# Kernel tuning notes

Hardware: AMD Instinct MI355X
Metric: run time of the kernel (lower is better)

## Reference

```python
import jax, jax.numpy as jnp
import numpy as np

E = 1024   # embedding_dim
H = 16     # num_head
D = 64     # dim_head (E == H*D)
R = 8      # LoRA rank
BATCH = 2
SEQ = 2048
EPS = 1e-6


def setup_inputs() -> dict:
    key = jax.random.key(0)
    ks = jax.random.split(key, 16)
    s = 0.02
    return {
        "y": jax.random.normal(ks[0], (BATCH, SEQ, E), jnp.float32),
        "Wqkv": jax.random.normal(ks[1], (3 * E, E), jnp.float32) * s,
        "bqkv": jax.random.normal(ks[2], (3 * E,), jnp.float32) * s,
        "Wmsa": jax.random.normal(ks[3], (E, E), jnp.float32) * s,
        "Bq": jax.random.normal(ks[4], (E, R), jnp.float32) * s,
        "Aq": jax.random.normal(ks[5], (R, E), jnp.float32) * s,
        "Bk": jax.random.normal(ks[6], (E, R), jnp.float32) * s,
        "Ak": jax.random.normal(ks[7], (R, E), jnp.float32) * s,
        "Bv": jax.random.normal(ks[8], (E, R), jnp.float32) * s,
        "Av": jax.random.normal(ks[9], (R, E), jnp.float32) * s,
        "Bo": jax.random.normal(ks[10], (E, R), jnp.float32) * s,
        "Ao": jax.random.normal(ks[11], (R, E), jnp.float32) * s,
        "gamma": jnp.ones((E,), jnp.float32),
        "beta": jnp.zeros((E,), jnp.float32),
        "i": 0,
    }


def reference(y, Wqkv, bqkv, Wmsa, Bq, Aq, Bk, Ak, Bv, Av, Bo, Ao, gamma, beta, i):
    B, S, En = y.shape
    # fused QKV projection: nn.Linear -> y @ W.T + b
    qkv = (y @ Wqkv.T + bqkv).reshape(B, S, 3, H, D).transpose(2, 0, 3, 1, 4)
    Q, K, V = qkv[0], qkv[1], qkv[2]          # each [B,H,S,D]

    def lora_delta(Bw, Aw):
        # torch: y @ (B.weight @ A.weight), reshaped to heads
        return (y @ (Bw @ Aw)).reshape(B, S, H, D).transpose(0, 2, 1, 3)

    Q = Q + lora_delta(Bq, Aq)
    K = K + lora_delta(Bk, Ak)
    V = V + lora_delta(Bv, Av)

    scale = jnp.asarray(np.sqrt(D), y.dtype)
    scores = jnp.einsum('bhqd,bhkd->bhqk', Q, K) / scale
    attn = jax.nn.softmax(scores, axis=-1)
    o = jnp.einsum('bhqk,bhkd->bhqd', attn, V)          # [B,H,S,D]
    o = o.transpose(0, 2, 1, 3).reshape(B, S, H * D)    # [B,S,E]

    msa = o @ Wmsa.T + o @ (Bo @ Ao)
    res = msa + y

    mu = jnp.mean(res, axis=-1, keepdims=True)
    var = jnp.var(res, axis=-1, keepdims=True)
    return (res - mu) * jax.lax.rsqrt(var + EPS) * gamma + beta
```

## Files before the change

kernel.cpp:

```cpp
#include <hip/hip_runtime.h>
#include <hip/hip_bf16.h>
#include <stdint.h>

typedef __attribute__((ext_vector_type(8))) short short8;
typedef __attribute__((ext_vector_type(4))) float f32x4;

typedef const __attribute__((address_space(1))) void gv_t;
typedef __attribute__((address_space(3))) void lv_t;

#define SCQ 0.18033688011112042f

__device__ __forceinline__ void gl_lds16(const void* g, void* l) {
    __builtin_amdgcn_global_load_lds((gv_t*)g, (lv_t*)l, 16, 0, 0);
}

__device__ __forceinline__ unsigned short f2bf(float f) {
    union { float f; unsigned int u; } v; v.f = f;
    unsigned int r = v.u + 0x7fffu + ((v.u >> 16) & 1u);
    return (unsigned short)(r >> 16);
}

__device__ __forceinline__ unsigned int pack2bf(float a, float b) {
    union { __hip_bfloat162 h2; unsigned int u; } cv;
    cv.h2 = __float22bfloat162_rn(make_float2(a, b));
    return cv.u;
}

__device__ __forceinline__ f32x4 zero4() { f32x4 z = {0.f, 0.f, 0.f, 0.f}; return z; }

__global__ void k_prep(const float* __restrict__ y,
                       const float* __restrict__ Wqkv, const float* __restrict__ Wmsa,
                       const float* __restrict__ Bq, const float* __restrict__ Aq,
                       const float* __restrict__ Bk, const float* __restrict__ Ak,
                       const float* __restrict__ Bv, const float* __restrict__ Av,
                       const float* __restrict__ Bo, const float* __restrict__ Ao,
                       unsigned short* __restrict__ wout, unsigned short* __restrict__ yb) {
    const int bid = blockIdx.x;
    if (bid < 16384) {
        int idx = bid * 256 + threadIdx.x;
        int n = idx >> 10, k = idx & 1023;
        int sel = n >> 10, n0 = n & 1023;
        const float* Bp = (sel == 0) ? Bq : (sel == 1) ? Bk : (sel == 2) ? Bv : Bo;
        const float* Ap = (sel == 0) ? Aq : (sel == 1) ? Ak : (sel == 2) ? Av : Ao;
        float acc = (sel < 3) ? Wqkv[idx] : Wmsa[idx - 3145728];
        #pragma unroll
        for (int r = 0; r < 8; ++r) acc += Bp[k * 8 + r] * Ap[r * 1024 + n0];
        wout[idx] = f2bf(acc * ((sel == 0) ? SCQ : 1.0f));
    } else {
        int i = ((bid - 16384) * 256 + threadIdx.x) * 4;
        float4 v = *(const float4*)(y + i);
        union { unsigned short u[4]; uint2 w; } o;
        o.u[0] = f2bf(v.x); o.u[1] = f2bf(v.y); o.u[2] = f2bf(v.z); o.u[3] = f2bf(v.w);
        *(uint2*)(yb + i) = o.w;
    }
}

template <int TM, int EPI, int MINW>
__global__ __launch_bounds__(256, MINW) void k_gemm(const unsigned short* __restrict__ Ag,
                                                    const unsigned short* __restrict__ Bg,
                                                    const float* __restrict__ bias,
                                                    const float* __restrict__ yres,
                                                    unsigned short* __restrict__ vtg,
                                                    void* __restrict__ Cout,
                                                    int M, int N, int K) {
    constexpr int WAVES_N = 256 / TM;
    constexpr int WN = TM / 2;
    constexpr int NI = WN / 16;
    constexpr int ACALLS = TM / 64;
    __shared__ unsigned short As[2][TM * 32];
    __shared__ unsigned short Bs[2][128 * 32];
    const int flat = threadIdx.x;
    const int m0 = blockIdx.y * TM, n0 = blockIdx.x * 128;
    const int lane = flat & 63, wave = flat >> 6;
    const int l16 = lane & 15, quad = lane >> 4;
    const int wm = (wave / WAVES_N) * 64, wn = (wave % WAVES_N) * WN;

    f32x4 acc[4][NI];
    #pragma unroll
    for (int mi = 0; mi < 4; ++mi)
        #pragma unroll
        for (int ni = 0; ni < NI; ++ni) acc[mi][ni] = zero4();

    const unsigned short* ap = Ag + (size_t)(m0 + (flat >> 2)) * K + (flat & 3) * 8;
    const unsigned short* bp = Bg + (size_t)(n0 + (flat >> 2)) * K + (flat & 3) * 8;
    const size_t rstep = (size_t)64 * K;

    #pragma unroll
    for (int c = 0; c < ACALLS; ++c) gl_lds16(ap + c * rstep, &As[0][c * 2048 + flat * 8]);
    gl_lds16(bp,         &Bs[0][flat * 8]);
    gl_lds16(bp + rstep, &Bs[0][2048 + flat * 8]);
    ap += 32; bp += 32;
    __syncthreads();

    for (int k0 = 0; k0 < K; k0 += 32) {
        const int cur = (k0 >> 5) & 1;
        if (k0 + 32 < K) {
            const int nxt = cur ^ 1;
            #pragma unroll
            for (int c = 0; c < ACALLS; ++c) gl_lds16(ap + c * rstep, &As[nxt][c * 2048 + flat * 8]);
            gl_lds16(bp,         &Bs[nxt][flat * 8]);
            gl_lds16(bp + rstep, &Bs[nxt][2048 + flat * 8]);
            ap += 32; bp += 32;
        }

        short8 af[4], bfr[NI];
        #pragma unroll
        for (int i = 0; i < 4; ++i) af[i] = *(const short8*)&As[cur][(wm + i * 16 + l16) * 32 + quad * 8];
        #pragma unroll
        for (int i = 0; i < NI; ++i) bfr[i] = *(const short8*)&Bs[cur][(wn + i * 16 + l16) * 32 + quad * 8];
        #pragma unroll
        for (int mi = 0; mi < 4; ++mi)
            #pragma unroll
            for (int ni = 0; ni < NI; ++ni)
                acc[mi][ni] = __builtin_amdgcn_mfma_f32_16x16x32_bf16(af[mi], bfr[ni], acc[mi][ni], 0, 0, 0);

        __syncthreads();
    }

    if (EPI == 0) {
        unsigned short* C = (unsigned short*)Cout;
        if (n0 < 2048) {
            #pragma unroll
            for (int ni = 0; ni < NI; ++ni) {
                int col = n0 + wn + ni * 16 + l16;
                float bv = bias[col] * ((col < 1024) ? SCQ : 1.0f);
                #pragma unroll
                for (int mi = 0; mi < 4; ++mi) {
                    int row = m0 + wm + mi * 16 + quad * 4;
                    #pragma unroll
                    for (int r = 0; r < 4; ++r)
                        C[(size_t)(row + r) * N + col] = f2bf(acc[mi][ni][r] + bv);
                }
            }
        } else {
            #pragma unroll
            for (int ni = 0; ni < NI; ++ni) {
                int col = n0 + wn + ni * 16 + l16;
                float bv = bias[col];
                int hh = (col - 2048) >> 6, dd = col & 63;
                unsigned short* vrow0 = vtg + (size_t)(hh * 64 + dd) * 2048;
                #pragma unroll
                for (int mi = 0; mi < 4; ++mi) {
                    int row = m0 + wm + mi * 16 + quad * 4;
                    int bb = row >> 11, ss = row & 2047;
                    uint2 w;
                    w.x = pack2bf(acc[mi][ni][0] + bv, acc[mi][ni][1] + bv);
                    w.y = pack2bf(acc[mi][ni][2] + bv, acc[mi][ni][3] + bv);
                    *(uint2*)(vrow0 + (size_t)bb * 2097152 + ss) = w;
                }
            }
        }
    } else {
        float* C = (float*)Cout;
        #pragma unroll
        for (int ni = 0; ni < NI; ++ni) {
            int col = n0 + wn + ni * 16 + l16;
            #pragma unroll
            for (int mi = 0; mi < 4; ++mi) {
                int row = m0 + wm + mi * 16 + quad * 4;
                #pragma unroll
                for (int r = 0; r < 4; ++r)
                    C[(size_t)(row + r) * N + col] = acc[mi][ni][r] + yres[(size_t)(row + r) * N + col];
            }
        }
    }
}

__global__ __launch_bounds__(256, 3) void k_attn(const unsigned short* __restrict__ qkv,
                                                 const unsigned short* __restrict__ vtg,
                                                 unsigned short* __restrict__ o) {
    __shared__ unsigned short LDS[24576];
    unsigned short* Qs = LDS;
    unsigned short* Ks0 = LDS + 8192;
    unsigned short* Vt0 = LDS + 16384;

    const int t = threadIdx.x;
    const int lane = t & 63, wave = t >> 6;
    const int l16 = lane & 15, quad = lane >> 4;
    const int l8 = l16 & 7;
    const int q0 = blockIdx.x * 128;
    const int h = blockIdx.y, b = blockIdx.z;

    const unsigned short* qbase = qkv + (size_t)(b * 2048) * 3072 + h * 64;
    const unsigned short* kbase = qbase + 1024;
    const unsigned short* vtbase = vtg + (size_t)((b * 16 + h) * 64) * 2048;

    #pragma unroll
    for (int i = 0; i < 4; ++i) {
        int B = i * 256 + t;
        int row = B >> 3, c = (B & 7) ^ (row & 7);
        gl_lds16(qbase + (size_t)(q0 + row) * 3072 + c * 8, &Qs[B * 8]);
    }

    const int B0 = t, B1 = t + 256;
    const int r0 = B0 >> 3, c0 = (B0 & 7) ^ (r0 & 7);
    const int r1 = B1 >> 3, c1 = (B1 & 7) ^ (r1 & 7);
    const unsigned short* kp0 = kbase + (size_t)r0 * 3072 + c0 * 8;
    const unsigned short* kp1 = kbase + (size_t)r1 * 3072 + c1 * 8;
    const unsigned short* vp0 = vtbase + (size_t)r0 * 2048 + c0 * 8;
    const unsigned short* vp1 = vtbase + (size_t)r1 * 2048 + c1 * 8;

    gl_lds16(kp0, &Ks0[B0 * 8]);
    gl_lds16(kp1, &Ks0[B1 * 8]);
    gl_lds16(vp0, &Vt0[B0 * 8]);
    gl_lds16(vp1, &Vt0[B1 * 8]);
    kp0 += 64 * 3072; kp1 += 64 * 3072; vp0 += 64; vp1 += 64;

    __syncthreads();

    short8 qf[2][2];
    #pragma unroll
    for (int ni = 0; ni < 2; ++ni)
        #pragma unroll
        for (int kk = 0; kk < 2; ++kk)
            qf[ni][kk] = *(const short8*)&Qs[(wave * 32 + ni * 16 + l16) * 64 + ((kk * 4 + quad) ^ l8) * 8];

    f32x4 acc_o[2][4];
    #pragma unroll
    for (int mo = 0; mo < 2; ++mo)
        #pragma unroll
        for (int nd = 0; nd < 4; ++nd) acc_o[mo][nd] = zero4();
    f32x4 acc_l[2] = {zero4(), zero4()};
    short8 ones;
    #pragma unroll
    for (int i = 0; i < 8; ++i) ones[i] = (short)0x3F80;

    for (int j = 0; j < 32; ++j) {
        const unsigned short* Ks = Ks0 + (j & 1) * 4096;
        const unsigned short* Vt = Vt0 + (j & 1) * 4096;

        if (j < 31) {
            unsigned short* Kn = Ks0 + ((j + 1) & 1) * 4096;
            unsigned short* Vn = Vt0 + ((j + 1) & 1) * 4096;
            gl_lds16(kp0, &Kn[B0 * 8]);
            gl_lds16(kp1, &Kn[B1 * 8]);
            gl_lds16(vp0, &Vn[B0 * 8]);
            gl_lds16(vp1, &Vn[B1 * 8]);
            kp0 += 64 * 3072; kp1 += 64 * 3072; vp0 += 64; vp1 += 64;
        }

        f32x4 sacc[4][2];
        #pragma unroll
        for (int mi = 0; mi < 4; ++mi)
            #pragma unroll
            for (int ni = 0; ni < 2; ++ni) sacc[mi][ni] = zero4();
        #pragma unroll
        for (int kk = 0; kk < 2; ++kk)
            #pragma unroll
            for (int mi = 0; mi < 4; ++mi) {
                short8 kf = *(const short8*)&Ks[(mi * 16 + l16) * 64 + ((kk * 4 + quad) ^ l8) * 8];
                #pragma unroll
                for (int ni = 0; ni < 2; ++ni)
                    sacc[mi][ni] = __builtin_amdgcn_mfma_f32_16x16x32_bf16(kf, qf[ni][kk], sacc[mi][ni], 0, 0, 0);
            }

        short8 pf[2][2];
        #pragma unroll
        for (int ni = 0; ni < 2; ++ni)
            #pragma unroll
            for (int kk = 0; kk < 2; ++kk) {
                float e00 = __builtin_amdgcn_exp2f(sacc[2 * kk][ni][0]);
                float e01 = __builtin_amdgcn_exp2f(sacc[2 * kk][ni][1]);
                float e02 = __builtin_amdgcn_exp2f(sacc[2 * kk][ni][2]);
                float e03 = __builtin_amdgcn_exp2f(sacc[2 * kk][ni][3]);
                float e10 = __builtin_amdgcn_exp2f(sacc[2 * kk + 1][ni][0]);
                float e11 = __builtin_amdgcn_exp2f(sacc[2 * kk + 1][ni][1]);
                float e12 = __builtin_amdgcn_exp2f(sacc[2 * kk + 1][ni][2]);
                float e13 = __builtin_amdgcn_exp2f(sacc[2 * kk + 1][ni][3]);
                unsigned int a0 = pack2bf(e00, e01);
                unsigned int b0 = pack2bf(e10, e11);
                unsigned int a1 = pack2bf(e02, e03);
                unsigned int b1 = pack2bf(e12, e13);
                asm volatile("v_permlane32_swap_b32 %0, %1\n\t"
                             "v_permlane16_swap_b32 %0, %1"
                             : "+v"(a0), "+v"(b0));
                asm volatile("v_permlane32_swap_b32 %0, %1\n\t"
                             "v_permlane16_swap_b32 %0, %1"
                             : "+v"(a1), "+v"(b1));
                union { unsigned int u[4]; short8 s; } cv;
                cv.u[0] = a0; cv.u[1] = a1; cv.u[2] = b0; cv.u[3] = b1;
                pf[ni][kk] = cv.s;
            }

        #pragma unroll
        for (int kk = 0; kk < 2; ++kk) {
            #pragma unroll
            for (int mo = 0; mo < 2; ++mo)
                acc_l[mo] = __builtin_amdgcn_mfma_f32_16x16x32_bf16(pf[mo][kk], ones, acc_l[mo], 0, 0, 0);
            #pragma unroll
            for (int nd = 0; nd < 4; ++nd) {
                short8 vf = *(const short8*)&Vt[(nd * 16 + l16) * 64 + ((kk * 4 + quad) ^ l8) * 8];
                #pragma unroll
                for (int mo = 0; mo < 2; ++mo)
                    acc_o[mo][nd] = __builtin_amdgcn_mfma_f32_16x16x32_bf16(pf[mo][kk], vf, acc_o[mo][nd], 0, 0, 0);
            }
        }

        __syncthreads();
    }

    #pragma unroll
    for (int mo = 0; mo < 2; ++mo)
        #pragma unroll
        for (int rr = 0; rr < 4; ++rr) {
            float inv = 1.0f / acc_l[mo][rr];
            int qg = q0 + wave * 32 + mo * 16 + quad * 4 + rr;
            size_t base = ((size_t)(b * 2048 + qg)) * 1024 + h * 64;
            #pragma unroll
            for (int nd = 0; nd < 4; ++nd)
                o[base + nd * 16 + l16] = f2bf(acc_o[mo][nd][rr] * inv);
        }
}

__global__ __launch_bounds__(256) void k_ln(const float* __restrict__ res,
                                            const float* __restrict__ g,
                                            const float* __restrict__ be,
                                            float* __restrict__ out) {
    __shared__ float red[8];
    const int row = blockIdx.x, t = threadIdx.x;
    const float* x = res + (size_t)row * 1024;
    float4 v = *(const float4*)(x + t * 4);
    float s = v.x + v.y + v.z + v.w;
    float sq = v.x * v.x + v.y * v.y + v.z * v.z + v.w * v.w;
    #pragma unroll
    for (int off = 32; off; off >>= 1) { s += __shfl_down(s, off); sq += __shfl_down(sq, off); }
    if ((t & 63) == 0) { red[t >> 6] = s; red[4 + (t >> 6)] = sq; }
    __syncthreads();
    float ts = red[0] + red[1] + red[2] + red[3];
    float tq = red[4] + red[5] + red[6] + red[7];
    float mu = ts * (1.f / 1024.f);
    float var = tq * (1.f / 1024.f) - mu * mu;
    float rstd = rsqrtf(var + 1e-6f);
    float4 gg = *(const float4*)(g + t * 4);
    float4 bb = *(const float4*)(be + t * 4);
    float4 ov;
    ov.x = (v.x - mu) * rstd * gg.x + bb.x;
    ov.y = (v.y - mu) * rstd * gg.y + bb.y;
    ov.z = (v.z - mu) * rstd * gg.z + bb.z;
    ov.w = (v.w - mu) * rstd * gg.w + bb.w;
    *(float4*)(out + (size_t)row * 1024 + t * 4) = ov;
}

extern "C" void kernel_launch(void* const* d_in, const int* in_sizes, int n_in,
                              void* d_out, int out_size, void* d_ws, size_t ws_size,
                              hipStream_t stream) {
    (void)in_sizes; (void)n_in; (void)out_size; (void)ws_size;
    const float* y    = (const float*)d_in[0];
    const float* Wqkv = (const float*)d_in[1];
    const float* bqkv = (const float*)d_in[2];
    const float* Wmsa = (const float*)d_in[3];
    const float* Bq = (const float*)d_in[4];
    const float* Aq = (const float*)d_in[5];
    const float* Bk = (const float*)d_in[6];
    const float* Ak = (const float*)d_in[7];
    const float* Bv = (const float*)d_in[8];
    const float* Av = (const float*)d_in[9];
    const float* Bo = (const float*)d_in[10];
    const float* Ao = (const float*)d_in[11];
    const float* gamma = (const float*)d_in[12];
    const float* beta  = (const float*)d_in[13];

    char* ws = (char*)d_ws;
    unsigned short* yb   = (unsigned short*)(ws);
    unsigned short* weq  = (unsigned short*)(ws + (8u  << 20));
    unsigned short* qkv  = (unsigned short*)(ws + (16u << 20));
    unsigned short* vtg  = (unsigned short*)(ws + (40u << 20));
    unsigned short* wem  = weq + 3145728;
    unsigned short* obuf = yb;
    float* res = (float*)qkv;

    k_prep<<<17408, 256, 0, stream>>>(y, Wqkv, Wmsa, Bq, Aq, Bk, Ak, Bv, Av, Bo, Ao, weq, yb);
    k_gemm<128, 0, 3><<<dim3(24, 32), 256, 0, stream>>>(yb, weq, bqkv, nullptr, vtg, (void*)qkv, 4096, 3072, 1024);
    k_attn<<<dim3(16, 16, 2), 256, 0, stream>>>(qkv, vtg, obuf);
    k_gemm<64, 1, 4><<<dim3(8, 64), 256, 0, stream>>>(obuf, wem, nullptr, y, nullptr, (void*)res, 4096, 1024, 1024);
    k_ln  <<<4096, 256, 0, stream>>>(res, gamma, beta, (float*)d_out);
}
```

Baseline: 212.5 us.

## Split attention over two KV halves and add a partial-output reduction kernel

The attention kernel now splits the key/value sequence into two halves across extra blocks, doubling the grid. It frees LDS by reusing the Q staging area for K buffers and raises the occupancy hint from 3 to 4 blocks. Each split writes unnormalized bf16 partial outputs plus row sums, which a new reduction kernel adds, normalizes and writes out. The goal is better CU utilization at this small grid size. The cost is an extra launch, extra global traffic, and bf16 rounding of the unnormalized partial outputs.

After: 215.6 us. No clear change (+1.5%).

```diff
diff --git a/kernel.cpp b/kernel.cpp
--- a/kernel.cpp
+++ b/kernel.cpp
@@ -18,6 +18,10 @@
     union { float f; unsigned int u; } v; v.f = f;
     unsigned int r = v.u + 0x7fffu + ((v.u >> 16) & 1u);
     return (unsigned short)(r >> 16);
+}
+
+__device__ __forceinline__ float bf2f(unsigned short u) {
+    union { unsigned int i; float f; } v; v.i = ((unsigned int)u) << 16; return v.f;
 }
 
 __device__ __forceinline__ unsigned int pack2bf(float a, float b) {
@@ -166,24 +170,26 @@
     }
 }
 
-__global__ __launch_bounds__(256, 3) void k_attn(const unsigned short* __restrict__ qkv,
+__global__ __launch_bounds__(256, 4) void k_attn(const unsigned short* __restrict__ qkv,
                                                  const unsigned short* __restrict__ vtg,
-                                                 unsigned short* __restrict__ o) {
-    __shared__ unsigned short LDS[24576];
+                                                 unsigned short* __restrict__ opart,
+                                                 float* __restrict__ lout) {
+    __shared__ unsigned short LDS[16384];
     unsigned short* Qs = LDS;
-    unsigned short* Ks0 = LDS + 8192;
-    unsigned short* Vt0 = LDS + 16384;
+    unsigned short* Ks0 = LDS;
+    unsigned short* Vt0 = LDS + 8192;
 
     const int t = threadIdx.x;
     const int lane = t & 63, wave = t >> 6;
     const int l16 = lane & 15, quad = lane >> 4;
     const int l8 = l16 & 7;
     const int q0 = blockIdx.x * 128;
-    const int h = blockIdx.y, b = blockIdx.z;
+    const int h = blockIdx.y;
+    const int b = blockIdx.z >> 1, split = blockIdx.z & 1;
 
     const unsigned short* qbase = qkv + (size_t)(b * 2048) * 3072 + h * 64;
-    const unsigned short* kbase = qbase + 1024;
-    const unsigned short* vtbase = vtg + (size_t)((b * 16 + h) * 64) * 2048;
+    const unsigned short* kbase = qbase + 1024 + (size_t)(split * 1024) * 3072;
+    const unsigned short* vtbase = vtg + (size_t)((b * 16 + h) * 64) * 2048 + split * 1024;
 
     #pragma unroll
     for (int i = 0; i < 4; ++i) {
@@ -200,21 +206,23 @@
     const unsigned short* vp0 = vtbase + (size_t)r0 * 2048 + c0 * 8;
     const unsigned short* vp1 = vtbase + (size_t)r1 * 2048 + c1 * 8;
 
+    __syncthreads();
+
+    short8 qf[2][2];
+    #pragma unroll
+    for (int ni = 0; ni < 2; ++ni)
+        #pragma unroll
+        for (int kk = 0; kk < 2; ++kk)
+            qf[ni][kk] = *(const short8*)&Qs[(wave * 32 + ni * 16 + l16) * 64 + ((kk * 4 + quad) ^ l8) * 8];
+
+    __syncthreads();
+
     gl_lds16(kp0, &Ks0[B0 * 8]);
     gl_lds16(kp1, &Ks0[B1 * 8]);
     gl_lds16(vp0, &Vt0[B0 * 8]);
     gl_lds16(vp1, &Vt0[B1 * 8]);
     kp0 += 64 * 3072; kp1 += 64 * 3072; vp0 += 64; vp1 += 64;
 
-    __syncthreads();
-
-    short8 qf[2][2];
-    #pragma unroll
-    for (int ni = 0; ni < 2; ++ni)
-        #pragma unroll
-        for (int kk = 0; kk < 2; ++kk)
-            qf[ni][kk] = *(const short8*)&Qs[(wave * 32 + ni * 16 + l16) * 64 + ((kk * 4 + quad) ^ l8) * 8];
-
     f32x4 acc_o[2][4];
     #pragma unroll
     for (int mo = 0; mo < 2; ++mo)
@@ -225,11 +233,13 @@
     #pragma unroll
     for (int i = 0; i < 8; ++i) ones[i] = (short)0x3F80;
 
-    for (int j = 0; j < 32; ++j) {
+    __syncthreads();
+
+    for (int j = 0; j < 16; ++j) {
         const unsigned short* Ks = Ks0 + (j & 1) * 4096;
         const unsigned short* Vt = Vt0 + (j & 1) * 4096;
 
-        if (j < 31) {
+        if (j < 15) {
             unsigned short* Kn = Ks0 + ((j + 1) & 1) * 4096;
             unsigned short* Vn = Vt0 + ((j + 1) & 1) * 4096;
             gl_lds16(kp0, &Kn[B0 * 8]);
@@ -299,17 +309,43 @@
         __syncthreads();
     }
 
+    const size_t obase = ((size_t)(split * 32 + b * 16 + h)) * 2048;
     #pragma unroll
     for (int mo = 0; mo < 2; ++mo)
         #pragma unroll
         for (int rr = 0; rr < 4; ++rr) {
-            float inv = 1.0f / acc_l[mo][rr];
             int qg = q0 + wave * 32 + mo * 16 + quad * 4 + rr;
-            size_t base = ((size_t)(b * 2048 + qg)) * 1024 + h * 64;
+            unsigned short* op = opart + (obase + qg) * 64;
             #pragma unroll
             for (int nd = 0; nd < 4; ++nd)
-                o[base + nd * 16 + l16] = f2bf(acc_o[mo][nd][rr] * inv);
-        }
+                op[nd * 16 + l16] = f2bf(acc_o[mo][nd][rr]);
+            if (l16 == 0)
+                lout[(size_t)(b * 2048 + qg) * 1536 + 1024 + split * 16 + h] = acc_l[mo][rr];
+        }
+}
+
+__global__ __launch_bounds__(256) void k_ored(const unsigned short* __restrict__ opart,
+                                              const float* __restrict__ lin,
+                                              unsigned short* __restrict__ o) {
+    const int bid = blockIdx.x;
+    const int bh = bid >> 7, chunk = bid & 127;
+    const int t = threadIdx.x;
+    const int qloc = t >> 4, dd = (t & 15) * 4;
+    const int q = chunk * 16 + qloc;
+    const int b = bh >> 4, h = bh & 15;
+    const size_t i0 = ((size_t)bh * 2048 + q) * 64 + dd;
+    const size_t i1 = ((size_t)(32 + bh) * 2048 + q) * 64 + dd;
+    uint2 p0 = *(const uint2*)(opart + i0);
+    uint2 p1 = *(const uint2*)(opart + i1);
+    const size_t lrow = (size_t)(b * 2048 + q) * 1536 + 1024;
+    float inv = 1.0f / (lin[lrow + h] + lin[lrow + 16 + h]);
+    union { uint2 w; unsigned short u[4]; } a, c;
+    a.w = p0;
+    union { uint2 w; unsigned short u[4]; } bb; bb.w = p1;
+    #pragma unroll
+    for (int i = 0; i < 4; ++i)
+        c.u[i] = f2bf((bf2f(a.u[i]) + bf2f(bb.u[i])) * inv);
+    *(uint2*)(o + ((size_t)(b * 2048 + q)) * 1024 + h * 64 + dd) = c.w;
 }
 
 __global__ __launch_bounds__(256) void k_ln(const float* __restrict__ res,
@@ -365,13 +401,15 @@
     unsigned short* weq  = (unsigned short*)(ws + (8u  << 20));
     unsigned short* qkv  = (unsigned short*)(ws + (16u << 20));
     unsigned short* vtg  = (unsigned short*)(ws + (40u << 20));
+    unsigned short* opart= (unsigned short*)(ws + (48u << 20));
     unsigned short* wem  = weq + 3145728;
     unsigned short* obuf = yb;
     float* res = (float*)qkv;
 
     k_prep<<<17408, 256, 0, stream>>>(y, Wqkv, Wmsa, Bq, Aq, Bk, Ak, Bv, Av, Bo, Ao, weq, yb);
     k_gemm<128, 0, 3><<<dim3(24, 32), 256, 0, stream>>>(yb, weq, bqkv, nullptr, vtg, (void*)qkv, 4096, 3072, 1024);
-    k_attn<<<dim3(16, 16, 2), 256, 0, stream>>>(qkv, vtg, obuf);
+    k_attn<<<dim3(16, 16, 4), 256, 0, stream>>>(qkv, vtg, opart, (float*)qkv);
+    k_ored<<<4096, 256, 0, stream>>>(opart, (const float*)qkv, obuf);
     k_gemm<64, 1, 4><<<dim3(8, 64), 256, 0, stream>>>(obuf, wem, nullptr, y, nullptr, (void*)res, 4096, 1024, 1024);
     k_ln  <<<4096, 256, 0, stream>>>(res, gamma, beta, (float*)d_out);
 }
```
